# Kernel tuning notes

Hardware: AMD Instinct MI355X
Metric: run time of the kernel (lower is better)

Reference implementation:

```python
import jax, jax.numpy as jnp
import numpy as np

EPS = 1e-8


def setup_inputs() -> dict:
    key = jax.random.key(0)
    ks = jax.random.split(key, 8)
    B, N, D = 8, 2048, 768
    H, R = 768, 4
    return {
        "x": jax.random.normal(ks[0], (B, N, D), dtype=jnp.float32),
        "scale": jnp.ones((D,), dtype=jnp.float32),
        "U": jax.random.normal(ks[1], (H, R), dtype=jnp.float32) * 0.02,
        "V": jax.random.normal(ks[2], (H, R), dtype=jnp.float32) * 0.02,
        "S_param": jax.random.normal(ks[3], (H, H), dtype=jnp.float32) * 0.01,
        "Bm": jax.random.normal(ks[4], (H, D), dtype=jnp.float32) * (1.0 / np.sqrt(D)),
        "Cm": jax.random.normal(ks[5], (D, H), dtype=jnp.float32) * (1.0 / np.sqrt(H)),
        "gate_w": jax.random.normal(ks[6], (D, D), dtype=jnp.float32) * (1.0 / np.sqrt(D)),
        "gate_b": jnp.zeros((D,), dtype=jnp.float32),
        "alpha": jnp.full((1,), 0.1, dtype=jnp.float32),
    }


def reference(x, scale, U, V, S_param, Bm, Cm, gate_w, gate_b, alpha):
    B, N, D = x.shape
    H = Bm.shape[0]
    # A = diag(A_diag) + U V^T + (S - S^T); A_diag is a fixed buffer.
    A_diag = -jnp.linspace(1.0, float(H), H, dtype=x.dtype) / H
    A = jnp.diag(A_diag) + U @ V.T + (S_param - S_param.T)
    At = A.T  # apply as h @ A.T
    # RMSNorm
    rms = jnp.sqrt(jnp.mean(x * x, axis=-1, keepdims=True) + EPS)
    xn = x / rms * scale
    # Precompute input injections u_t = x_t @ B.T for all t: (N, B, H)
    u = jnp.einsum('bnd,hd->nbh', xn, Bm)

    def step(h, ut):
        h = h @ At + ut
        return h, h @ Cm.T  # (B, D)

    h0 = jnp.zeros((B, H), dtype=x.dtype)
    _, y_fwd = jax.lax.scan(step, h0, u)                 # (N, B, D)
    _, y_bwd = jax.lax.scan(step, h0, u, reverse=True)   # (N, B, D), indexed in time order
    y = 0.5 * (y_fwd + y_bwd)
    y = jnp.swapaxes(y, 0, 1)  # (B, N, D)
    # Gate
    g = jax.nn.sigmoid(jnp.einsum('bnd,ed->bne', xn, gate_w) + gate_b)
    y = y * g
    # Skip (dropout is identity in eval)
    return x + alpha * y
```

## Files before the change

kernel.cpp:

```cpp
#include <hip/hip_runtime.h>


typedef short  bfrag __attribute__((ext_vector_type(8)));
typedef float  ffrag __attribute__((ext_vector_type(4)));
typedef float  f4    __attribute__((ext_vector_type(4)));
typedef short  s4v   __attribute__((ext_vector_type(4)));

#define DEV static __device__ __forceinline__
#define Hn 768
#define FLS 132
#define BLS 260

DEV unsigned short f2bf(float f) {
  unsigned u = __float_as_uint(f);
  u += 0x7fffu + ((u >> 16) & 1u);
  return (unsigned short)(u >> 16);
}
DEV float bf2f(unsigned short s) { return __uint_as_float(((unsigned)s) << 16); }

DEV ffrag mfma16(bfrag a, bfrag b, ffrag c) {
  return __builtin_amdgcn_mfma_f32_16x16x32_bf16(a, b, c, 0, 0, 0);
}

DEV void glds16(const unsigned short* g, unsigned short* l) {
  __builtin_amdgcn_global_load_lds(
      (const __attribute__((address_space(1))) unsigned int*)g,
      (__attribute__((address_space(3))) unsigned int*)l, 16, 0, 0);
}

union BF8 { bfrag v; unsigned short u[8]; };

__global__ __launch_bounds__(256) void k_abuild(
    const float* __restrict__ U, const float* __restrict__ V,
    const float* __restrict__ S, const float* __restrict__ Bm,
    const float* __restrict__ Cm, const float* __restrict__ gw,
    float* __restrict__ Af, float* __restrict__ AfT,
    unsigned short* __restrict__ Abf,
    unsigned short* __restrict__ Bmb, unsigned short* __restrict__ Cmb,
    unsigned short* __restrict__ gwb, unsigned short* __restrict__ zp) {
  int i = blockIdx.x;
  int task = blockIdx.y;
  if (task == 0) {
    float u0 = U[i*4+0], u1 = U[i*4+1], u2 = U[i*4+2], u3 = U[i*4+3];
    for (int j = threadIdx.x; j < Hn; j += 256) {
      float a = u0*V[j*4+0] + u1*V[j*4+1] + u2*V[j*4+2] + u3*V[j*4+3]
              + S[i*Hn+j] - S[j*Hn+i];
      if (i == j) a += -(float)(i+1) / 768.0f;
      Af[i*Hn+j]  = a;
      AfT[j*Hn+i] = a;
      Abf[i*Hn+j] = f2bf(a);
    }
    if (i == 0) for (int j = threadIdx.x; j < 1024; j += 256) zp[j] = 0;
  } else {
    const float* src = (task==1) ? Bm : (task==2) ? Cm : gw;
    unsigned short* dst = (task==1) ? Bmb : (task==2) ? Cmb : gwb;
    for (int j = threadIdx.x; j < Hn; j += 256) dst[i*Hn+j] = f2bf(src[i*Hn+j]);
  }
}

__global__ __launch_bounds__(256) void k_rms(
    const float* __restrict__ x, const float* __restrict__ scale,
    unsigned short* __restrict__ xn) {
  int row  = blockIdx.x * 4 + (threadIdx.x >> 6);
  int lane = threadIdx.x & 63;
  int b = row >> 11, t = row & 2047;
  const float* xr = x + (long)row * Hn;
  float v[12];
  float ss = 0.f;
#pragma unroll
  for (int j = 0; j < 12; ++j) { v[j] = xr[lane + j*64]; ss += v[j]*v[j]; }
#pragma unroll
  for (int off = 1; off < 64; off <<= 1) ss += __shfl_xor(ss, off);
  float inv = 1.0f / sqrtf(ss / 768.0f + 1e-8f);
  unsigned short* dst = xn + ((long)t * 8 + b) * Hn;
#pragma unroll
  for (int j = 0; j < 12; ++j) dst[lane + j*64] = f2bf(v[j] * inv * scale[lane + j*64]);
}

__global__ __launch_bounds__(512) void k_sq(
    const float* __restrict__ X, const float* __restrict__ XT,
    float* __restrict__ Z, float* __restrict__ ZT,
    unsigned short* __restrict__ Zbf) {
  int tid = threadIdx.x, lane = tid & 63, w = tid >> 6;
  int mw = w >> 2, nw = w & 3, l15 = lane & 15, lhi = lane >> 4;
  int rb = blockIdx.x * 64, cb = blockIdx.y * 128;
  ffrag acc[2][2] = {};
  for (int kt = 0; kt < 24; ++kt) {
    int k0 = kt*32 + lhi*8;
    BF8 ah[2], al[2], bh[2], bl[2];
#pragma unroll
    for (int mt = 0; mt < 2; ++mt) {
      const f4* p = (const f4*)(X + (long)(rb + mw*32 + mt*16 + l15) * Hn + k0);
      f4 x0 = p[0], x1 = p[1];
#pragma unroll
      for (int j = 0; j < 8; ++j) {
        float f = (j < 4) ? x0[j] : x1[j-4];
        unsigned short h = f2bf(f);
        ah[mt].u[j] = h; al[mt].u[j] = f2bf(f - bf2f(h));
      }
    }
#pragma unroll
    for (int nt = 0; nt < 2; ++nt) {
      const f4* p = (const f4*)(XT + (long)(cb + nw*32 + nt*16 + l15) * Hn + k0);
      f4 x0 = p[0], x1 = p[1];
#pragma unroll
      for (int j = 0; j < 8; ++j) {
        float f = (j < 4) ? x0[j] : x1[j-4];
        unsigned short h = f2bf(f);
        bh[nt].u[j] = h; bl[nt].u[j] = f2bf(f - bf2f(h));
      }
    }
#pragma unroll
    for (int mt = 0; mt < 2; ++mt)
#pragma unroll
      for (int nt = 0; nt < 2; ++nt) {
        acc[mt][nt] = mfma16(ah[mt].v, bh[nt].v, acc[mt][nt]);
        acc[mt][nt] = mfma16(ah[mt].v, bl[nt].v, acc[mt][nt]);
        acc[mt][nt] = mfma16(al[mt].v, bh[nt].v, acc[mt][nt]);
      }
  }
#pragma unroll
  for (int mt = 0; mt < 2; ++mt)
#pragma unroll
    for (int nt = 0; nt < 2; ++nt)
#pragma unroll
      for (int q = 0; q < 4; ++q) {
        int grow = rb + mw*32 + mt*16 + lhi*4 + q;
        int gcol = cb + nw*32 + nt*16 + l15;
        float vv = acc[mt][nt][q];
        Z[(long)grow*Hn + gcol] = vv;
        ZT[(long)gcol*Hn + grow] = vv;
        Zbf[(long)grow*Hn + gcol] = f2bf(vv);
      }
}

__global__ __launch_bounds__(256) void k_lvl(
    const unsigned short* __restrict__ A0s, const unsigned short* __restrict__ B0s,
    const unsigned short* __restrict__ res, unsigned short* __restrict__ outb,
    const unsigned short* __restrict__ zp, int sh) {
  __shared__ __align__(16) unsigned short ldsb[2 * 8192];

  const int tid = threadIdx.x, lane = tid & 63, w = tid >> 6;
  const int l15 = lane & 15, lhi = lane >> 4;
  const int wr = w >> 1, wc = w & 1;

  const int nwg = gridDim.x;
  const int q8 = nwg >> 3, r8 = nwg & 7, xcd = blockIdx.x & 7, fo = blockIdx.x >> 3;
  const int wg = (xcd < r8 ? xcd*(q8+1) : r8*(q8+1) + (xcd - r8)*q8) + fo;
  const int cb = wg % 6, rbk = wg / 6;
  const long r0  = (long)rbk * 128;
  const long bc0 = (long)cb * 128;
  const int dir = (r0 >= 16384) ? 1 : 0;
  const bool skip = dir ? (r0 >= 32768 - sh) : (r0 + 128 <= sh);

  const int rowin = lane >> 2, ch = lane & 3;
  long gA[2]; bool vA[2]; long gB[2]; int lbase[2];
#pragma unroll
  for (int jj = 0; jj < 2; ++jj) {
    const int inst = w*2 + jj;
    const int r = inst*16 + rowin;
    const int c = ch ^ ((r ^ (r >> 2)) & 3);
    lbase[jj] = inst * 512;
    long gr = r0 + r + (dir ? sh : -sh);
    vA[jj] = dir ? (gr < 32768) : (gr >= 0);
    gA[jj] = gr * Hn + c*8;
    gB[jj] = (bc0 + r) * Hn + c*8;
  }

  auto stage = [&](int buf, int kt) {
    const int ko = kt * 32;
    unsigned short* dst = ldsb + buf * 8192;
#pragma unroll
    for (int jj = 0; jj < 2; ++jj) {
      const unsigned short* g = vA[jj] ? (A0s + gA[jj] + ko) : zp;
      glds16(g, dst + lbase[jj]);
      glds16(B0s + gB[jj] + ko, dst + 4096 + lbase[jj]);
    }
  };

  ffrag acc[4][4] = {};
  const int cx = (lhi ^ ((l15 ^ (l15 >> 2)) & 3)) * 8;

  if (!skip) {
    stage(0, 0);
    __syncthreads();
    int cur = 0;
    for (int kt = 0; kt < 24; ++kt) {
      if (kt < 23) stage(cur ^ 1, kt + 1);
      const unsigned short* L = ldsb + cur * 8192;
      bfrag a[4], b[4];
#pragma unroll
      for (int mt = 0; mt < 4; ++mt)
        a[mt] = *(const bfrag*)&L[(wr*64 + mt*16 + l15)*32 + cx];
#pragma unroll
      for (int nt = 0; nt < 4; ++nt)
        b[nt] = *(const bfrag*)&L[4096 + (wc*64 + nt*16 + l15)*32 + cx];
#pragma unroll
      for (int mt = 0; mt < 4; ++mt)
#pragma unroll
        for (int nt = 0; nt < 4; ++nt)
          acc[mt][nt] = mfma16(a[mt], b[nt], acc[mt][nt]);
      __syncthreads();
      cur ^= 1;
    }
  }

  float* fl = (float*)ldsb;
#pragma unroll
  for (int p = 0; p < 4; ++p) {
    __syncthreads();
    if (wr == (p >> 1)) {
#pragma unroll
      for (int mt2 = 0; mt2 < 2; ++mt2) {
        const int mt = (p & 1)*2 + mt2;
#pragma unroll
        for (int nt = 0; nt < 4; ++nt)
#pragma unroll
          for (int q = 0; q < 4; ++q)
            fl[(mt2*16 + lhi*4 + q)*FLS + wc*64 + nt*16 + l15] = acc[mt][nt][q];
      }
    }
    __syncthreads();
    for (int i = tid; i < 1024; i += 256) {
      const int row = i >> 5;
      const int cc  = (i & 31) << 2;
      f4 v = *(const f4*)&fl[row*FLS + cc];
      const long grow = r0 + p*32 + row;
      const long gcol = bc0 + cc;
      const long go = grow * Hn + gcol;
      s4v rv = *(const s4v*)&res[go];
#pragma unroll
      for (int j = 0; j < 4; ++j) v[j] += bf2f(((unsigned short*)&rv)[j]);
      s4v ov;
#pragma unroll
      for (int j = 0; j < 4; ++j) ((unsigned short*)&ov)[j] = f2bf(v[j]);
      *(s4v*)&outb[go] = ov;
    }
  }
}

__global__ __launch_bounds__(512) void k_cmb(
    const unsigned short* __restrict__ A0s, const unsigned short* __restrict__ B0s,
    const unsigned short* __restrict__ res, unsigned short* __restrict__ outb,
    const unsigned short* __restrict__ zp, int sh) {
  constexpr int BUFS = 2 * 4096 + 8192;
  __shared__ __align__(16) unsigned short ldsb[2 * BUFS];

  const int tid = threadIdx.x, lane = tid & 63, w = tid >> 6;
  const int l15 = lane & 15, lhi = lane >> 4;
  const int wr = w >> 2, wc = w & 3;

  const int nwg = gridDim.x;
  const int q8 = nwg >> 3, r8 = nwg & 7, xcd = blockIdx.x & 7, fo = blockIdx.x >> 3;
  const int wg = (xcd < r8 ? xcd*(q8+1) : r8*(q8+1) + (xcd - r8)*q8) + fo;
  const int cb = wg % 3, rbk = wg / 3;
  const long r0  = (long)rbk * 128;
  const long bc0 = (long)cb * 256;

  const int rowin = lane >> 2, ch = lane & 3;
  const int rA = w*16 + rowin;
  const int cswz = ch ^ ((rowin ^ (rowin >> 2)) & 3);
  long gA[2]; bool vA[2];
  { long g0 = r0 + rA - sh;         vA[0] = (g0 >= 0);    gA[0] = g0 * Hn + cswz*8; }
  { long g1 = r0 + rA + 16384 + sh; vA[1] = (g1 < 32768); gA[1] = g1 * Hn + cswz*8; }
  long gB[2];
#pragma unroll
  for (int j = 0; j < 2; ++j)
    gB[j] = (bc0 + j*128 + rA) * Hn + cswz*8;

  auto stage = [&](int buf, int kt) {
    const int ko = kt * 32;
    unsigned short* dst = ldsb + buf * BUFS;
#pragma unroll
    for (int s = 0; s < 2; ++s) {
      const unsigned short* g = vA[s] ? (A0s + gA[s] + ko) : zp;
      glds16(g, dst + s*4096 + w*512);
    }
#pragma unroll
    for (int j = 0; j < 2; ++j)
      glds16(B0s + gB[j] + ko, dst + 2*4096 + j*4096 + w*512);
  };

  ffrag acc[4][4] = {};
  const int cx = (lhi ^ ((l15 ^ (l15 >> 2)) & 3)) * 8;

  stage(0, 0);
  __syncthreads();
  int cur = 0;
  for (int kt = 0; kt < 24; ++kt) {
    if (kt < 23) stage(cur ^ 1, kt + 1);
    const unsigned short* L = ldsb + cur * BUFS;
    bfrag a[2][4], b[4];
#pragma unroll
    for (int mt = 0; mt < 4; ++mt) {
      const int row = wr*64 + mt*16 + l15;
      a[0][mt] = *(const bfrag*)&L[row*32 + cx];
      a[1][mt] = *(const bfrag*)&L[4096 + row*32 + cx];
    }
#pragma unroll
    for (int nt = 0; nt < 4; ++nt) {
      const int row = wc*64 + nt*16 + l15;
      b[nt] = *(const bfrag*)&L[2*4096 + row*32 + cx];
    }
#pragma unroll
    for (int mt = 0; mt < 4; ++mt)
#pragma unroll
      for (int nt = 0; nt < 4; ++nt) {
        acc[mt][nt] = mfma16(a[0][mt], b[nt], acc[mt][nt]);
        acc[mt][nt] = mfma16(a[1][mt], b[nt], acc[mt][nt]);
      }
    __syncthreads();
    cur ^= 1;
  }

  float* fl = (float*)ldsb;
#pragma unroll
  for (int p = 0; p < 4; ++p) {
    __syncthreads();
#pragma unroll
    for (int nt = 0; nt < 4; ++nt)
#pragma unroll
      for (int q = 0; q < 4; ++q)
        fl[(wr*16 + lhi*4 + q)*BLS + wc*64 + nt*16 + l15] = acc[p][nt][q];
    __syncthreads();
    for (int i = tid; i < 2048; i += 512) {
      const int srow = i >> 6;
      const int cc   = (i & 63) << 2;
      f4 v = *(const f4*)&fl[srow*BLS + cc];
      const long grow = r0 + (srow >> 4)*64 + p*16 + (srow & 15);
      const long gcol = bc0 + cc;
      const long go = grow * Hn + gcol;
      s4v ra = *(const s4v*)&res[go];
      s4v rb2 = *(const s4v*)&res[go + (long)16384*Hn];
#pragma unroll
      for (int j = 0; j < 4; ++j)
        v[j] += bf2f(((unsigned short*)&ra)[j]) + bf2f(((unsigned short*)&rb2)[j]);
      s4v ov;
#pragma unroll
      for (int j = 0; j < 4; ++j) ((unsigned short*)&ov)[j] = f2bf(v[j]);
      *(s4v*)&outb[go] = ov;
    }
  }
}

__global__ __launch_bounds__(256) void k_uz(
    const unsigned short* __restrict__ xn, const unsigned short* __restrict__ Bmb,
    const unsigned short* __restrict__ gwb,
    unsigned short* __restrict__ u, unsigned short* __restrict__ z) {
  __shared__ __align__(16) unsigned short ldsb[2 * 3 * 4096];

  const int tid = threadIdx.x, lane = tid & 63, w = tid >> 6;
  const int l15 = lane & 15, lhi = lane >> 4;
  const int wr = w >> 1, wc = w & 1;

  const int nwg = gridDim.x;
  const int q8 = nwg >> 3, r8 = nwg & 7, xcd = blockIdx.x & 7, fo = blockIdx.x >> 3;
  const int wg = (xcd < r8 ? xcd*(q8+1) : r8*(q8+1) + (xcd - r8)*q8) + fo;
  const int cb = wg % 6, rbk = wg / 6;
  const long r0 = (long)rbk * 128;
  const long bc0 = (long)cb * 128;

  const int rowin = lane >> 2, ch = lane & 3;
  long gA[2]; long gB[2]; int lbase[2];
#pragma unroll
  for (int jj = 0; jj < 2; ++jj) {
    const int inst = w*2 + jj;
    const int r = inst*16 + rowin;
    const int c = ch ^ ((r ^ (r >> 2)) & 3);
    lbase[jj] = inst * 512;
    gA[jj] = (r0 + r) * Hn + c*8;
    gB[jj] = (bc0 + r) * Hn + c*8;
  }

  auto stage = [&](int buf, int kt) {
    const int ko = kt * 32;
    unsigned short* dst = ldsb + buf * 12288;
#pragma unroll
    for (int jj = 0; jj < 2; ++jj) {
      glds16(xn  + gA[jj] + ko, dst + 0*4096 + lbase[jj]);
      glds16(Bmb + gB[jj] + ko, dst + 1*4096 + lbase[jj]);
      glds16(gwb + gB[jj] + ko, dst + 2*4096 + lbase[jj]);
    }
  };

  ffrag acc[4][4] = {};
  ffrag accZ[4][4] = {};
  const int cx = (lhi ^ ((l15 ^ (l15 >> 2)) & 3)) * 8;

  stage(0, 0);
  __syncthreads();
  int cur = 0;
  for (int kt = 0; kt < 24; ++kt) {
    if (kt < 23) stage(cur ^ 1, kt + 1);
    const unsigned short* L = ldsb + cur * 12288;
    bfrag a[4], b0[4], b1[4];
#pragma unroll
    for (int mt = 0; mt < 4; ++mt)
      a[mt] = *(const bfrag*)&L[(wr*64 + mt*16 + l15)*32 + cx];
#pragma unroll
    for (int nt = 0; nt < 4; ++nt) {
      const int row = wc*64 + nt*16 + l15;
      b0[nt] = *(const bfrag*)&L[1*4096 + row*32 + cx];
      b1[nt] = *(const bfrag*)&L[2*4096 + row*32 + cx];
    }
#pragma unroll
    for (int mt = 0; mt < 4; ++mt)
#pragma unroll
      for (int nt = 0; nt < 4; ++nt) {
        acc[mt][nt]  = mfma16(a[mt], b0[nt], acc[mt][nt]);
        accZ[mt][nt] = mfma16(a[mt], b1[nt], accZ[mt][nt]);
      }
    __syncthreads();
    cur ^= 1;
  }

  float* fl = (float*)ldsb;
#pragma unroll
  for (int which = 0; which < 2; ++which) {
#pragma unroll
    for (int hh = 0; hh < 2; ++hh) {
      __syncthreads();
      if (wr == hh) {
#pragma unroll
        for (int mt = 0; mt < 4; ++mt)
#pragma unroll
          for (int nt = 0; nt < 4; ++nt)
#pragma unroll
            for (int q = 0; q < 4; ++q)
              fl[(mt*16 + lhi*4 + q)*FLS + wc*64 + nt*16 + l15] =
                  which ? accZ[mt][nt][q] : acc[mt][nt][q];
      }
      __syncthreads();
      for (int i = tid; i < 2048; i += 256) {
        const int row = i >> 5;
        const int cc  = (i & 31) << 2;
        f4 v = *(const f4*)&fl[row*FLS + cc];
        const long go = (r0 + hh*64 + row) * Hn + bc0 + cc;
        s4v ov;
#pragma unroll
        for (int j = 0; j < 4; ++j) ((unsigned short*)&ov)[j] = f2bf(v[j]);
        if (which == 0) {
          *(s4v*)&u[go] = ov;
          *(s4v*)&u[go + (long)16384*Hn] = ov;
        } else {
          *(s4v*)&z[go] = ov;
        }
      }
    }
  }
}

__global__ __launch_bounds__(256) void k_fin2(
    const unsigned short* __restrict__ A0s, const unsigned short* __restrict__ B0s,
    const unsigned short* __restrict__ z,
    const float* __restrict__ gb, const float* __restrict__ alpha,
    const float* __restrict__ x, float* __restrict__ outf) {
  __shared__ __align__(16) unsigned short ldsb[2 * 8192];

  const int tid = threadIdx.x, lane = tid & 63, w = tid >> 6;
  const int l15 = lane & 15, lhi = lane >> 4;
  const int wr = w >> 1, wc = w & 1;

  const int nwg = gridDim.x;
  const int q8 = nwg >> 3, r8 = nwg & 7, xcd = blockIdx.x & 7, fo = blockIdx.x >> 3;
  const int wg = (xcd < r8 ? xcd*(q8+1) : r8*(q8+1) + (xcd - r8)*q8) + fo;
  const int cb = wg % 6, rbk = wg / 6;
  const long r0 = (long)rbk * 128;
  const long bc0 = (long)cb * 128;

  const int rowin = lane >> 2, ch = lane & 3;
  long gA[2]; long gB[2]; int lbase[2];
#pragma unroll
  for (int jj = 0; jj < 2; ++jj) {
    const int inst = w*2 + jj;
    const int r = inst*16 + rowin;
    const int c = ch ^ ((r ^ (r >> 2)) & 3);
    lbase[jj] = inst * 512;
    gA[jj] = (r0 + r) * Hn + c*8;
    gB[jj] = (bc0 + r) * Hn + c*8;
  }

  auto stage = [&](int buf, int kt) {
    const int ko = kt * 32;
    unsigned short* dst = ldsb + buf * 8192;
#pragma unroll
    for (int jj = 0; jj < 2; ++jj) {
      glds16(A0s + gA[jj] + ko, dst + lbase[jj]);
      glds16(B0s + gB[jj] + ko, dst + 4096 + lbase[jj]);
    }
  };

  ffrag acc[4][4] = {};
  const int cx = (lhi ^ ((l15 ^ (l15 >> 2)) & 3)) * 8;

  stage(0, 0);
  __syncthreads();
  int cur = 0;
  for (int kt = 0; kt < 24; ++kt) {
    if (kt < 23) stage(cur ^ 1, kt + 1);
    const unsigned short* L = ldsb + cur * 8192;
    bfrag a[4], b[4];
#pragma unroll
    for (int mt = 0; mt < 4; ++mt)
      a[mt] = *(const bfrag*)&L[(wr*64 + mt*16 + l15)*32 + cx];
#pragma unroll
    for (int nt = 0; nt < 4; ++nt)
      b[nt] = *(const bfrag*)&L[4096 + (wc*64 + nt*16 + l15)*32 + cx];
#pragma unroll
    for (int mt = 0; mt < 4; ++mt)
#pragma unroll
      for (int nt = 0; nt < 4; ++nt)
        acc[mt][nt] = mfma16(a[mt], b[nt], acc[mt][nt]);
    __syncthreads();
    cur ^= 1;
  }

  const float al = alpha[0];
  float* fl = (float*)ldsb;
#pragma unroll
  for (int p = 0; p < 4; ++p) {
    __syncthreads();
    if (wr == (p >> 1)) {
#pragma unroll
      for (int mt2 = 0; mt2 < 2; ++mt2) {
        const int mt = (p & 1)*2 + mt2;
#pragma unroll
        for (int nt = 0; nt < 4; ++nt)
#pragma unroll
          for (int q = 0; q < 4; ++q)
            fl[(mt2*16 + lhi*4 + q)*FLS + wc*64 + nt*16 + l15] = acc[mt][nt][q];
      }
    }
    __syncthreads();
    for (int i = tid; i < 1024; i += 256) {
      const int row = i >> 5;
      const int cc  = (i & 31) << 2;
      f4 v = *(const f4*)&fl[row*FLS + cc];
      const long grow = r0 + p*32 + row;
      const long gcol = bc0 + cc;
      const long go = grow * Hn + gcol;
      s4v zv = *(const s4v*)&z[go];
      f4 gbv = *(const f4*)&gb[gcol];
      const long t = grow >> 3, b = grow & 7;
      const long o = (b*2048 + t)*Hn + gcol;
      f4 xv = *(const f4*)&x[o];
      f4 ov;
#pragma unroll
      for (int j = 0; j < 4; ++j) {
        float zz = bf2f(((unsigned short*)&zv)[j]) + gbv[j];
        float g = 1.0f / (1.0f + __expf(-zz));
        ov[j] = xv[j] + al * 0.5f * v[j] * g;
      }
      *(f4*)&outf[o] = ov;
    }
  }
}

extern "C" void kernel_launch(void* const* d_in, const int* in_sizes, int n_in,
                              void* d_out, int out_size, void* d_ws, size_t ws_size,
                              hipStream_t stream) {
  const float* x     = (const float*)d_in[0];
  const float* scale = (const float*)d_in[1];
  const float* U     = (const float*)d_in[2];
  const float* V     = (const float*)d_in[3];
  const float* S     = (const float*)d_in[4];
  const float* Bm    = (const float*)d_in[5];
  const float* Cm    = (const float*)d_in[6];
  const float* gw    = (const float*)d_in[7];
  const float* gb    = (const float*)d_in[8];
  const float* alpha = (const float*)d_in[9];
  float* out = (float*)d_out;

  char* p = (char*)d_ws;
  auto alloc = [&](size_t sz) { char* r = p; p += (sz + 255) & ~(size_t)255; return r; };

  const size_t SZ_X  = (size_t)32768 * Hn * sizeof(unsigned short);
  const size_t SZ_BF = (size_t)16384 * Hn * sizeof(unsigned short);
  const size_t SZ_M  = (size_t)Hn * Hn * sizeof(float);
  const size_t SZ_MB = (size_t)Hn * Hn * sizeof(unsigned short);

  unsigned short* xn   = (unsigned short*)alloc(SZ_BF);
  unsigned short* zbuf = (unsigned short*)alloc(SZ_BF);
  unsigned short* XA = (unsigned short*)alloc(SZ_X);
  unsigned short* XB = (unsigned short*)alloc(SZ_X);
  float* Af  = (float*)alloc(SZ_M);
  float* AfT = (float*)alloc(SZ_M);
  float* P1  = (float*)alloc(SZ_M);
  float* P1T = (float*)alloc(SZ_M);
  float* P2  = (float*)alloc(SZ_M);
  float* P2T = (float*)alloc(SZ_M);
  unsigned short* Abf = (unsigned short*)alloc(SZ_MB);
  unsigned short* Ab[10];
  for (int i = 0; i < 10; ++i) Ab[i] = (unsigned short*)alloc(SZ_MB);
  unsigned short* Bmb = (unsigned short*)alloc(SZ_MB);
  unsigned short* Cmb = (unsigned short*)alloc(SZ_MB);
  unsigned short* gwb = (unsigned short*)alloc(SZ_MB);
  unsigned short* zp  = (unsigned short*)alloc(1024 * sizeof(unsigned short));

  if ((size_t)(p - (char*)d_ws) > ws_size) return;

  k_abuild<<<dim3(768, 4), 256, 0, stream>>>(U, V, S, Bm, Cm, gw,
      Af, AfT, Abf, Bmb, Cmb, gwb, zp);
  k_rms<<<4096, 256, 0, stream>>>(x, scale, xn);

  const float* sx = Af; const float* sxt = AfT;
  float* za = P1; float* zat = P1T; float* zb = P2; float* zbt = P2T;
  for (int i = 0; i < 10; ++i) {
    k_sq<<<dim3(12, 6), 512, 0, stream>>>(sx, sxt, za, zat, Ab[i]);
    sx = za; sxt = zat;
    float* t1 = za; float* t2 = zat; za = zb; zat = zbt; zb = t1; zbt = t2;
  }

  k_uz<<<768, 256, 0, stream>>>(xn, Bmb, gwb, XA, zbuf);

  unsigned short* src = XA; unsigned short* dst = XB;
  for (int i = 0; i < 10; ++i) {
    const unsigned short* W = (i == 0) ? Abf : Ab[i-1];
    k_lvl<<<1536, 256, 0, stream>>>(src, W, src, dst, zp, 8 << i);
    unsigned short* t = src; src = dst; dst = t;
  }
  k_cmb<<<384, 512, 0, stream>>>(src, Ab[9], src, XB, zp, 8192);

  k_fin2<<<768, 256, 0, stream>>>(XB, Cmb, zbuf, gb, alpha, x, out);
}
```

Before: 1.278 ms.

## Fuse first scan level into input projection and widen level-GEMM tiles

The first doubling level of the parallel scan is folded into the input-projection kernel. A precomputed W1 = A·B is used, so each row gets u_t plus u_{t∓8}·W1 in one GEMM pass, which removes one full k_lvl launch over the 32768x768 state. The level kernel is also retiled to 512 threads with 128x256 output tiles, so each A tile is loaded once per 256 columns and more data is reused per workgroup. This adds an extra small fp32 split-bf16 matmul and doubles the K work in the fused kernel, and it changes the rounding path for the first level.

```diff
diff --git a/kernel.cpp b/kernel.cpp
--- a/kernel.cpp
+++ b/kernel.cpp
@@ -36,8 +36,9 @@
     const float* __restrict__ Cm, const float* __restrict__ gw,
     float* __restrict__ Af, float* __restrict__ AfT,
     unsigned short* __restrict__ Abf,
-    unsigned short* __restrict__ Bmb, unsigned short* __restrict__ Cmb,
-    unsigned short* __restrict__ gwb, unsigned short* __restrict__ zp) {
+    unsigned short* __restrict__ Bmb, float* __restrict__ BmTf,
+    unsigned short* __restrict__ Cmb, unsigned short* __restrict__ gwb,
+    unsigned short* __restrict__ zp) {
   int i = blockIdx.x;
   int task = blockIdx.y;
   if (task == 0) {
@@ -51,9 +52,15 @@
       Abf[i*Hn+j] = f2bf(a);
     }
     if (i == 0) for (int j = threadIdx.x; j < 1024; j += 256) zp[j] = 0;
+  } else if (task == 1) {
+    for (int j = threadIdx.x; j < Hn; j += 256) {
+      float v = Bm[i*Hn+j];
+      Bmb[i*Hn+j]  = f2bf(v);
+      BmTf[(long)j*Hn+i] = v;
+    }
   } else {
-    const float* src = (task==1) ? Bm : (task==2) ? Cm : gw;
-    unsigned short* dst = (task==1) ? Bmb : (task==2) ? Cmb : gwb;
+    const float* src = (task==2) ? Cm : gw;
+    unsigned short* dst = (task==2) ? Cmb : gwb;
     for (int j = threadIdx.x; j < Hn; j += 256) dst[i*Hn+j] = f2bf(src[i*Hn+j]);
   }
 }
@@ -134,11 +141,70 @@
       }
 }
 
-__global__ __launch_bounds__(256) void k_lvl(
-    const unsigned short* __restrict__ A0s, const unsigned short* __restrict__ B0s,
-    const unsigned short* __restrict__ res, unsigned short* __restrict__ outb,
-    const unsigned short* __restrict__ zp, int sh) {
-  __shared__ __align__(16) unsigned short ldsb[2 * 8192];
+__global__ __launch_bounds__(512) void k_mul(
+    const float* __restrict__ X, const float* __restrict__ YT,
+    float* __restrict__ Z, float* __restrict__ ZT,
+    unsigned short* __restrict__ Zb) {
+  int tid = threadIdx.x, lane = tid & 63, w = tid >> 6;
+  int mw = w >> 2, nw = w & 3, l15 = lane & 15, lhi = lane >> 4;
+  int rb = blockIdx.x * 64, cb = blockIdx.y * 128;
+  ffrag acc[2][2] = {};
+  for (int kt = 0; kt < 24; ++kt) {
+    int k0 = kt*32 + lhi*8;
+    BF8 ah[2], al[2], bh[2], bl[2];
+#pragma unroll
+    for (int mt = 0; mt < 2; ++mt) {
+      const f4* p = (const f4*)(X + (long)(rb + mw*32 + mt*16 + l15) * Hn + k0);
+      f4 x0 = p[0], x1 = p[1];
+#pragma unroll
+      for (int j = 0; j < 8; ++j) {
+        float f = (j < 4) ? x0[j] : x1[j-4];
+        unsigned short h = f2bf(f);
+        ah[mt].u[j] = h; al[mt].u[j] = f2bf(f - bf2f(h));
+      }
+    }
+#pragma unroll
+    for (int nt = 0; nt < 2; ++nt) {
+      const f4* p = (const f4*)(YT + (long)(cb + nw*32 + nt*16 + l15) * Hn + k0);
+      f4 x0 = p[0], x1 = p[1];
+#pragma unroll
+      for (int j = 0; j < 8; ++j) {
+        float f = (j < 4) ? x0[j] : x1[j-4];
+        unsigned short h = f2bf(f);
+        bh[nt].u[j] = h; bl[nt].u[j] = f2bf(f - bf2f(h));
+      }
+    }
+#pragma unroll
+    for (int mt = 0; mt < 2; ++mt)
+#pragma unroll
+      for (int nt = 0; nt < 2; ++nt) {
+        acc[mt][nt] = mfma16(ah[mt].v, bh[nt].v, acc[mt][nt]);
+        acc[mt][nt] = mfma16(ah[mt].v, bl[nt].v, acc[mt][nt]);
+        acc[mt][nt] = mfma16(al[mt].v, bh[nt].v, acc[mt][nt]);
+      }
+  }
+#pragma unroll
+  for (int mt = 0; mt < 2; ++mt)
+#pragma unroll
+    for (int nt = 0; nt < 2; ++nt)
+#pragma unroll
+      for (int q = 0; q < 4; ++q) {
+        int grow = rb + mw*32 + mt*16 + lhi*4 + q;
+        int gcol = cb + nw*32 + nt*16 + l15;
+        float vv = acc[mt][nt][q];
+        if (Z)  Z[(long)grow*Hn + gcol] = vv;
+        if (ZT) ZT[(long)gcol*Hn + grow] = vv;
+        Zb[(long)grow*Hn + gcol] = f2bf(vv);
+      }
+}
+
+__global__ __launch_bounds__(256) void k_u2z(
+    const unsigned short* __restrict__ xn, const unsigned short* __restrict__ Bmb,
+    const unsigned short* __restrict__ W1b, const unsigned short* __restrict__ gwb,
+    unsigned short* __restrict__ X2, unsigned short* __restrict__ z,
+    const unsigned short* __restrict__ zp) {
+  constexpr int BUFS = 5 * 4096;
+  __shared__ __align__(16) unsigned short ldsb[2 * BUFS];
 
   const int tid = threadIdx.x, lane = tid & 63, w = tid >> 6;
   const int l15 = lane & 15, lhi = lane >> 4;
@@ -151,31 +217,157 @@
   const long r0  = (long)rbk * 128;
   const long bc0 = (long)cb * 128;
   const int dir = (r0 >= 16384) ? 1 : 0;
-  const bool skip = dir ? (r0 >= 32768 - sh) : (r0 + 128 <= sh);
+  const long r0m = r0 - (long)dir * 16384;
 
   const int rowin = lane >> 2, ch = lane & 3;
-  long gA[2]; bool vA[2]; long gB[2]; int lbase[2];
+  long gA0[2]; long gA1[2]; bool vA1[2]; long gB[2]; int lbase[2];
 #pragma unroll
   for (int jj = 0; jj < 2; ++jj) {
     const int inst = w*2 + jj;
     const int r = inst*16 + rowin;
     const int c = ch ^ ((r ^ (r >> 2)) & 3);
     lbase[jj] = inst * 512;
-    long gr = r0 + r + (dir ? sh : -sh);
-    vA[jj] = dir ? (gr < 32768) : (gr >= 0);
-    gA[jj] = gr * Hn + c*8;
-    gB[jj] = (bc0 + r) * Hn + c*8;
+    gA0[jj] = (r0m + r) * Hn + c*8;
+    long g1 = r0m + r + (dir ? 8 : -8);
+    vA1[jj] = (g1 >= 0) && (g1 < 16384);
+    gA1[jj] = g1 * Hn + c*8;
+    gB[jj]  = (bc0 + r) * Hn + c*8;
   }
 
   auto stage = [&](int buf, int kt) {
     const int ko = kt * 32;
-    unsigned short* dst = ldsb + buf * 8192;
+    unsigned short* dst = ldsb + buf * BUFS;
 #pragma unroll
     for (int jj = 0; jj < 2; ++jj) {
-      const unsigned short* g = vA[jj] ? (A0s + gA[jj] + ko) : zp;
-      glds16(g, dst + lbase[jj]);
-      glds16(B0s + gB[jj] + ko, dst + 4096 + lbase[jj]);
-    }
+      glds16(xn + gA0[jj] + ko, dst + 0*4096 + lbase[jj]);
+      glds16(vA1[jj] ? (xn + gA1[jj] + ko) : zp, dst + 1*4096 + lbase[jj]);
+      glds16(Bmb + gB[jj] + ko, dst + 2*4096 + lbase[jj]);
+      glds16(W1b + gB[jj] + ko, dst + 3*4096 + lbase[jj]);
+      glds16(gwb + gB[jj] + ko, dst + 4*4096 + lbase[jj]);
+    }
+  };
+
+  ffrag acc[4][4] = {};
+  ffrag accZ[4][4] = {};
+  const int cx = (lhi ^ ((l15 ^ (l15 >> 2)) & 3)) * 8;
+
+  stage(0, 0);
+  __syncthreads();
+  int cur = 0;
+  for (int kt = 0; kt < 24; ++kt) {
+    if (kt < 23) stage(cur ^ 1, kt + 1);
+    const unsigned short* L = ldsb + cur * BUFS;
+    bfrag a0[4], a1[4], b0[4], b1[4], b2[4];
+#pragma unroll
+    for (int mt = 0; mt < 4; ++mt) {
+      const int row = wr*64 + mt*16 + l15;
+      a0[mt] = *(const bfrag*)&L[0*4096 + row*32 + cx];
+      a1[mt] = *(const bfrag*)&L[1*4096 + row*32 + cx];
+    }
+#pragma unroll
+    for (int nt = 0; nt < 4; ++nt) {
+      const int row = wc*64 + nt*16 + l15;
+      b0[nt] = *(const bfrag*)&L[2*4096 + row*32 + cx];
+      b1[nt] = *(const bfrag*)&L[3*4096 + row*32 + cx];
+      b2[nt] = *(const bfrag*)&L[4*4096 + row*32 + cx];
+    }
+#pragma unroll
+    for (int mt = 0; mt < 4; ++mt)
+#pragma unroll
+      for (int nt = 0; nt < 4; ++nt) {
+        acc[mt][nt] = mfma16(a0[mt], b0[nt], acc[mt][nt]);
+        acc[mt][nt] = mfma16(a1[mt], b1[nt], acc[mt][nt]);
+      }
+    if (!dir) {
+#pragma unroll
+      for (int mt = 0; mt < 4; ++mt)
+#pragma unroll
+        for (int nt = 0; nt < 4; ++nt)
+          accZ[mt][nt] = mfma16(a0[mt], b2[nt], accZ[mt][nt]);
+    }
+    __syncthreads();
+    cur ^= 1;
+  }
+
+  float* fl = (float*)ldsb;
+#pragma unroll
+  for (int which = 0; which < 2; ++which) {
+    if (which == 1 && dir) break;
+#pragma unroll
+    for (int hh = 0; hh < 2; ++hh) {
+      __syncthreads();
+      if (wr == hh) {
+#pragma unroll
+        for (int mt = 0; mt < 4; ++mt)
+#pragma unroll
+          for (int nt = 0; nt < 4; ++nt)
+#pragma unroll
+            for (int q = 0; q < 4; ++q)
+              fl[(mt*16 + lhi*4 + q)*FLS + wc*64 + nt*16 + l15] =
+                  which ? accZ[mt][nt][q] : acc[mt][nt][q];
+      }
+      __syncthreads();
+      for (int i = tid; i < 2048; i += 256) {
+        const int row = i >> 5;
+        const int cc  = (i & 31) << 2;
+        f4 v = *(const f4*)&fl[row*FLS + cc];
+        s4v ov;
+#pragma unroll
+        for (int j = 0; j < 4; ++j) ((unsigned short*)&ov)[j] = f2bf(v[j]);
+        if (which == 0) {
+          const long go = (r0 + hh*64 + row) * Hn + bc0 + cc;
+          *(s4v*)&X2[go] = ov;
+        } else {
+          const long go = (r0m + hh*64 + row) * Hn + bc0 + cc;
+          *(s4v*)&z[go] = ov;
+        }
+      }
+    }
+  }
+}
+
+__global__ __launch_bounds__(512) void k_lvl(
+    const unsigned short* __restrict__ A0s, const unsigned short* __restrict__ B0s,
+    const unsigned short* __restrict__ res, unsigned short* __restrict__ outb,
+    const unsigned short* __restrict__ zp, int sh) {
+  constexpr int BUFS = 4096 + 8192;
+  __shared__ __align__(16) unsigned short ldsb[2 * BUFS];
+
+  const int tid = threadIdx.x, lane = tid & 63, w = tid >> 6;
+  const int l15 = lane & 15, lhi = lane >> 4;
+  const int wr = w >> 2, wc = w & 3;
+
+  const int nwg = gridDim.x;
+  const int q8 = nwg >> 3, r8 = nwg & 7, xcd = blockIdx.x & 7, fo = blockIdx.x >> 3;
+  const int wg = (xcd < r8 ? xcd*(q8+1) : r8*(q8+1) + (xcd - r8)*q8) + fo;
+  const int cb = wg % 3, rbk = wg / 3;
+  const long r0  = (long)rbk * 128;
+  const long bc0 = (long)cb * 256;
+  const int dir = (r0 >= 16384) ? 1 : 0;
+  const bool skip = dir ? (r0 >= 32768 - sh) : (r0 + 128 <= sh);
+
+  const int rowin = lane >> 2, ch = lane & 3;
+  const int rA = w*16 + rowin;
+  const int cswz = ch ^ ((rowin ^ (rowin >> 2)) & 3);
+  long gA; bool vA;
+  {
+    long gr = r0 + rA + (dir ? sh : -sh);
+    vA = dir ? (gr < 32768) : (gr >= 0);
+    gA = gr * Hn + cswz*8;
+  }
+  long gB[2];
+#pragma unroll
+  for (int j = 0; j < 2; ++j)
+    gB[j] = (bc0 + j*128 + rA) * Hn + cswz*8;
+
+  auto stage = [&](int buf, int kt) {
+    const int ko = kt * 32;
+    unsigned short* dst = ldsb + buf * BUFS;
+    const unsigned short* g = vA ? (A0s + gA + ko) : zp;
+    glds16(g, dst + w*512);
+#pragma unroll
+    for (int j = 0; j < 2; ++j)
+      glds16(B0s + gB[j] + ko, dst + 4096 + j*4096 + w*512);
   };
 
   ffrag acc[4][4] = {};
@@ -187,7 +379,7 @@
     int cur = 0;
     for (int kt = 0; kt < 24; ++kt) {
       if (kt < 23) stage(cur ^ 1, kt + 1);
-      const unsigned short* L = ldsb + cur * 8192;
+      const unsigned short* L = ldsb + cur * BUFS;
       bfrag a[4], b[4];
 #pragma unroll
       for (int mt = 0; mt < 4; ++mt)
@@ -209,23 +401,17 @@
 #pragma unroll
   for (int p = 0; p < 4; ++p) {
     __syncthreads();
-    if (wr == (p >> 1)) {
-#pragma unroll
-      for (int mt2 = 0; mt2 < 2; ++mt2) {
-        const int mt = (p & 1)*2 + mt2;
-#pragma unroll
-        for (int nt = 0; nt < 4; ++nt)
-#pragma unroll
-          for (int q = 0; q < 4; ++q)
-            fl[(mt2*16 + lhi*4 + q)*FLS + wc*64 + nt*16 + l15] = acc[mt][nt][q];
-      }
-    }
-    __syncthreads();
-    for (int i = tid; i < 1024; i += 256) {
-      const int row = i >> 5;
-      const int cc  = (i & 31) << 2;
-      f4 v = *(const f4*)&fl[row*FLS + cc];
-      const long grow = r0 + p*32 + row;
+#pragma unroll
+    for (int nt = 0; nt < 4; ++nt)
+#pragma unroll
+      for (int q = 0; q < 4; ++q)
+        fl[(wr*16 + lhi*4 + q)*BLS + wc*64 + nt*16 + l15] = acc[p][nt][q];
+    __syncthreads();
+    for (int i = tid; i < 2048; i += 512) {
+      const int srow = i >> 6;
+      const int cc   = (i & 63) << 2;
+      f4 v = *(const f4*)&fl[srow*BLS + cc];
+      const long grow = r0 + (srow >> 4)*64 + p*16 + (srow & 15);
       const long gcol = bc0 + cc;
       const long go = grow * Hn + gcol;
       s4v rv = *(const s4v*)&res[go];
@@ -339,113 +525,6 @@
 #pragma unroll
       for (int j = 0; j < 4; ++j) ((unsigned short*)&ov)[j] = f2bf(v[j]);
       *(s4v*)&outb[go] = ov;
-    }
-  }
-}
-
-__global__ __launch_bounds__(256) void k_uz(
-    const unsigned short* __restrict__ xn, const unsigned short* __restrict__ Bmb,
-    const unsigned short* __restrict__ gwb,
-    unsigned short* __restrict__ u, unsigned short* __restrict__ z) {
-  __shared__ __align__(16) unsigned short ldsb[2 * 3 * 4096];
-
-  const int tid = threadIdx.x, lane = tid & 63, w = tid >> 6;
-  const int l15 = lane & 15, lhi = lane >> 4;
-  const int wr = w >> 1, wc = w & 1;
-
-  const int nwg = gridDim.x;
-  const int q8 = nwg >> 3, r8 = nwg & 7, xcd = blockIdx.x & 7, fo = blockIdx.x >> 3;
-  const int wg = (xcd < r8 ? xcd*(q8+1) : r8*(q8+1) + (xcd - r8)*q8) + fo;
-  const int cb = wg % 6, rbk = wg / 6;
-  const long r0 = (long)rbk * 128;
-  const long bc0 = (long)cb * 128;
-
-  const int rowin = lane >> 2, ch = lane & 3;
-  long gA[2]; long gB[2]; int lbase[2];
-#pragma unroll
-  for (int jj = 0; jj < 2; ++jj) {
-    const int inst = w*2 + jj;
-    const int r = inst*16 + rowin;
-    const int c = ch ^ ((r ^ (r >> 2)) & 3);
-    lbase[jj] = inst * 512;
-    gA[jj] = (r0 + r) * Hn + c*8;
-    gB[jj] = (bc0 + r) * Hn + c*8;
-  }
-
-  auto stage = [&](int buf, int kt) {
-    const int ko = kt * 32;
-    unsigned short* dst = ldsb + buf * 12288;
-#pragma unroll
-    for (int jj = 0; jj < 2; ++jj) {
-      glds16(xn  + gA[jj] + ko, dst + 0*4096 + lbase[jj]);
-      glds16(Bmb + gB[jj] + ko, dst + 1*4096 + lbase[jj]);
-      glds16(gwb + gB[jj] + ko, dst + 2*4096 + lbase[jj]);
-    }
-  };
-
-  ffrag acc[4][4] = {};
-  ffrag accZ[4][4] = {};
-  const int cx = (lhi ^ ((l15 ^ (l15 >> 2)) & 3)) * 8;
-
-  stage(0, 0);
-  __syncthreads();
-  int cur = 0;
-  for (int kt = 0; kt < 24; ++kt) {
-    if (kt < 23) stage(cur ^ 1, kt + 1);
-    const unsigned short* L = ldsb + cur * 12288;
-    bfrag a[4], b0[4], b1[4];
-#pragma unroll
-    for (int mt = 0; mt < 4; ++mt)
-      a[mt] = *(const bfrag*)&L[(wr*64 + mt*16 + l15)*32 + cx];
-#pragma unroll
-    for (int nt = 0; nt < 4; ++nt) {
-      const int row = wc*64 + nt*16 + l15;
-      b0[nt] = *(const bfrag*)&L[1*4096 + row*32 + cx];
-      b1[nt] = *(const bfrag*)&L[2*4096 + row*32 + cx];
-    }
-#pragma unroll
-    for (int mt = 0; mt < 4; ++mt)
-#pragma unroll
-      for (int nt = 0; nt < 4; ++nt) {
-        acc[mt][nt]  = mfma16(a[mt], b0[nt], acc[mt][nt]);
-        accZ[mt][nt] = mfma16(a[mt], b1[nt], accZ[mt][nt]);
-      }
-    __syncthreads();
-    cur ^= 1;
-  }
-
-  float* fl = (float*)ldsb;
-#pragma unroll
-  for (int which = 0; which < 2; ++which) {
-#pragma unroll
-    for (int hh = 0; hh < 2; ++hh) {
-      __syncthreads();
-      if (wr == hh) {
-#pragma unroll
-        for (int mt = 0; mt < 4; ++mt)
-#pragma unroll
-          for (int nt = 0; nt < 4; ++nt)
-#pragma unroll
-            for (int q = 0; q < 4; ++q)
-              fl[(mt*16 + lhi*4 + q)*FLS + wc*64 + nt*16 + l15] =
-                  which ? accZ[mt][nt][q] : acc[mt][nt][q];
-      }
-      __syncthreads();
-      for (int i = tid; i < 2048; i += 256) {
-        const int row = i >> 5;
-        const int cc  = (i & 31) << 2;
-        f4 v = *(const f4*)&fl[row*FLS + cc];
-        const long go = (r0 + hh*64 + row) * Hn + bc0 + cc;
-        s4v ov;
-#pragma unroll
-        for (int j = 0; j < 4; ++j) ((unsigned short*)&ov)[j] = f2bf(v[j]);
-        if (which == 0) {
-          *(s4v*)&u[go] = ov;
-          *(s4v*)&u[go + (long)16384*Hn] = ov;
-        } else {
-          *(s4v*)&z[go] = ov;
-        }
-      }
     }
   }
 }
@@ -595,31 +674,37 @@
   unsigned short* Bmb = (unsigned short*)alloc(SZ_MB);
   unsigned short* Cmb = (unsigned short*)alloc(SZ_MB);
   unsigned short* gwb = (unsigned short*)alloc(SZ_MB);
+  unsigned short* W1b = (unsigned short*)alloc(SZ_MB);
   unsigned short* zp  = (unsigned short*)alloc(1024 * sizeof(unsigned short));
 
+  float* BmTf = P2;
+
   if ((size_t)(p - (char*)d_ws) > ws_size) return;
 
   k_abuild<<<dim3(768, 4), 256, 0, stream>>>(U, V, S, Bm, Cm, gw,
-      Af, AfT, Abf, Bmb, Cmb, gwb, zp);
+      Af, AfT, Abf, Bmb, BmTf, Cmb, gwb, zp);
   k_rms<<<4096, 256, 0, stream>>>(x, scale, xn);
 
-  const float* sx = Af; const float* sxt = AfT;
-  float* za = P1; float* zat = P1T; float* zb = P2; float* zbt = P2T;
-  for (int i = 0; i < 10; ++i) {
+  k_sq<<<dim3(12, 6), 512, 0, stream>>>(Af, AfT, P1, P1T, Ab[0]);
+  k_mul<<<dim3(12, 6), 512, 0, stream>>>(Af, BmTf, nullptr, nullptr, W1b);
+
+  const float* sx = P1; const float* sxt = P1T;
+  float* za = P2; float* zat = P2T; float* zb = P1; float* zbt = P1T;
+  for (int i = 1; i < 10; ++i) {
     k_sq<<<dim3(12, 6), 512, 0, stream>>>(sx, sxt, za, zat, Ab[i]);
     sx = za; sxt = zat;
     float* t1 = za; float* t2 = zat; za = zb; zat = zbt; zb = t1; zbt = t2;
   }
 
-  k_uz<<<768, 256, 0, stream>>>(xn, Bmb, gwb, XA, zbuf);
+  k_u2z<<<1536, 256, 0, stream>>>(xn, Bmb, W1b, gwb, XA, zbuf, zp);
 
   unsigned short* src = XA; unsigned short* dst = XB;
-  for (int i = 0; i < 10; ++i) {
-    const unsigned short* W = (i == 0) ? Abf : Ab[i-1];
-    k_lvl<<<1536, 256, 0, stream>>>(src, W, src, dst, zp, 8 << i);
+  for (int i = 1; i < 10; ++i) {
+    k_lvl<<<768, 512, 0, stream>>>(src, Ab[i-1], src, dst, zp, 8 << i);
     unsigned short* t = src; src = dst; dst = t;
   }
-  k_cmb<<<384, 512, 0, stream>>>(src, Ab[9], src, XB, zp, 8192);
-
-  k_fin2<<<768, 256, 0, stream>>>(XB, Cmb, zbuf, gb, alpha, x, out);
-}
+  unsigned short* xsum = (src == XA) ? XB : XA;
+  k_cmb<<<384, 512, 0, stream>>>(src, Ab[9], src, xsum, zp, 8192);
+
+  k_fin2<<<768, 256, 0, stream>>>(xsum, Cmb, zbuf, gb, alpha, x, out);
+}
```

New measurement: 1.336 ms. 4.6% more time.
